# Kernel optimization log

Measured on AMD Instinct MI355X. Metric: run time of the kernel, lower is better.

## Reference

```python
import jax, jax.numpy as jnp
import numpy as np

P = 3          # graph partitions
CO = 64        # out_channels
KS = 9         # temporal kernel size (Gamma)
STRIDE = 1     # temporal stride
EPS = 1e-3     # keras BatchNormalization default epsilon


def setup_inputs() -> dict:
    key = jax.random.key(0)
    k1, k2, k3 = jax.random.split(key, 3)
    x = jax.random.normal(k1, (32, 64, 300, 25), dtype=jnp.float32)      # (N, C_in, L, V)
    A = jax.random.uniform(k2, (3, 25, 25), dtype=jnp.float32)           # (P, V, V)
    W = jax.random.normal(k3, (64, 192), dtype=jnp.float32) * 0.05       # (C_in, C_out*P)
    gamma = jnp.ones((64,), dtype=jnp.float32)
    beta = jnp.zeros((64,), dtype=jnp.float32)
    mean = jnp.zeros((64,), dtype=jnp.float32)
    var = jnp.ones((64,), dtype=jnp.float32)
    return {"x": x, "A": A, "W": W, "gamma": gamma, "beta": beta, "mean": mean, "var": var}


def _lt_matrix(L):
    # sum of shifted identities: lt[r, r + i*STRIDE] = 1 for i in [0, KS//STRIDE)
    lt = jnp.zeros((L, L), dtype=jnp.float32)
    for i in range(KS // STRIDE):
        lt = lt + jnp.eye(L, k=i * STRIDE, dtype=jnp.float32)
    return lt


def reference(x, A, W, gamma, beta, mean, var):
    N, C, L, V = x.shape
    res = x  # identity residual (in_channels == out_channels, stride == 1)
    # 1x1 conv: (N,C,L,V) x (C, CO*P) -> (N, CO*P, L, V); channel k = c*P + p (split into CO groups of P)
    y = jnp.einsum('nclv,ck->nklv', x, W)
    y = y.reshape(N, CO, P, L, V)  # (N, C_out, P, L, V)
    # partitioned graph matmul over joints: contract V with A[p]
    z = jnp.einsum('ncplv,pvw->ncplw', y, A)
    # temporal aggregation via handcrafted banded matrix, then sum over partitions
    lt = _lt_matrix(L)
    t = jnp.einsum('ncplv,lm->ncmv', z, lt)  # partition sum fused into einsum
    # BN (inference) over channel axis + ReLU
    inv = gamma / jnp.sqrt(var + EPS)
    xn = (t - mean[None, :, None, None]) * inv[None, :, None, None] + beta[None, :, None, None]
    xn = jax.nn.relu(xn)
    # residual add + final ReLU (dropout is identity at inference)
    return jax.nn.relu(xn + res)
```

## Files before the change

kernel.cpp:

```cpp
#include <hip/hip_runtime.h>
#include <cstdint>
#include <cstddef>

typedef short bf16x8 __attribute__((ext_vector_type(8)));
typedef float f32x4 __attribute__((ext_vector_type(4)));

#define EPS 1e-3f

__device__ __forceinline__ short f32_to_bf16s(float f) {
    union { float f; uint32_t u; } v; v.f = f;
    return (short)((v.u + 0x7FFFu + ((v.u >> 16) & 1u)) >> 16);
}

__global__ __launch_bounds__(256) void prep_kernel(const float* __restrict__ A,
                                                   const float* __restrict__ W,
                                                   unsigned short* __restrict__ wt,
                                                   unsigned short* __restrict__ at) {
    int idx = blockIdx.x * 256 + threadIdx.x;
    if (idx < 12288) {
        int kp = idx >> 6, ci = idx & 63;
        wt[idx] = (unsigned short)f32_to_bf16s(W[ci * 192 + kp]);
    } else {
        int j = idx - 12288;
        if (j < 3072) {
            int w = j / 96, k = j - w * 96;
            float val = 0.f;
            if (w < 25 && k < 75) {
                int p = k / 25, v = k - p * 25;
                val = A[(p * 25 + v) * 25 + w];
            }
            at[j] = (unsigned short)f32_to_bf16s(val);
        }
    }
}

__device__ __forceinline__ void do_group(int g, const unsigned short* __restrict__ wt,
    short* smem, const bf16x8 (&b1)[2][2], const bf16x8 (&b2)[2][3],
    const float* __restrict__ xn, float* __restrict__ outn,
    const float* scs, const float* shs,
    int lg, int wv, int q, int lcol)
{
    bf16x8 a1[3][2];
    #pragma unroll
    for (int mt = 0; mt < 3; ++mt)
        #pragma unroll
        for (int s = 0; s < 2; ++s)
            a1[mt][s] = *(const bf16x8*)(wt + (size_t)(g * 48 + mt * 16 + lcol) * 64 + 32 * s + 8 * q);

    f32x4 acc[3][2];
    #pragma unroll
    for (int mt = 0; mt < 3; ++mt)
        #pragma unroll
        for (int nt = 0; nt < 2; ++nt) acc[mt][nt] = (f32x4){0.f, 0.f, 0.f, 0.f};
    #pragma unroll
    for (int s = 0; s < 2; ++s)
        #pragma unroll
        for (int mt = 0; mt < 3; ++mt) {
            bf16x8 av = a1[mt][s];
            #pragma unroll
            for (int nt = 0; nt < 2; ++nt)
                acc[mt][nt] = __builtin_amdgcn_mfma_f32_16x16x32_bf16(av, b1[nt][s], acc[mt][nt], 0, 0, 0);
        }

    const size_t rbase = (size_t)lg * 25;
    float res[2][4];
    #pragma unroll
    for (int nt = 0; nt < 2; ++nt) {
        int w = nt * 16 + lcol;
        bool val = (w < 25) && (lg < 300);
        #pragma unroll
        for (int r = 0; r < 4; ++r) {
            int c = g * 16 + 4 * q + r;
            res[nt][r] = val ? xn[rbase + (size_t)c * 7500 + w] : 0.f;
        }
    }

    #pragma unroll
    for (int mt = 0; mt < 3; ++mt)
        #pragma unroll
        for (int nt = 0; nt < 2; ++nt) {
            int v = nt * 16 + lcol;
            if (v < 25) {
                #pragma unroll
                for (int r = 0; r < 4; ++r) {
                    int kpl = mt * 16 + 4 * q + r;
                    int cl = kpl / 3, p = kpl - 3 * cl;
                    smem[(wv * 16 + cl) * 104 + 25 * p + v] = f32_to_bf16s(acc[mt][nt][r]);
                }
            }
        }

    f32x4 c0 = {0.f, 0.f, 0.f, 0.f}, c1 = {0.f, 0.f, 0.f, 0.f};
    #pragma unroll
    for (int s = 0; s < 3; ++s) {
        bf16x8 a2 = *(const bf16x8*)&smem[(wv * 16 + lcol) * 104 + 32 * s + 8 * q];
        c0 = __builtin_amdgcn_mfma_f32_16x16x32_bf16(a2, b2[0][s], c0, 0, 0, 0);
        c1 = __builtin_amdgcn_mfma_f32_16x16x32_bf16(a2, b2[1][s], c1, 0, 0, 0);
    }

    if (lg < 300) {
        #pragma unroll
        for (int nt = 0; nt < 2; ++nt) {
            int w = nt * 16 + lcol;
            if (w < 25) {
                f32x4 cc = nt ? c1 : c0;
                #pragma unroll
                for (int r = 0; r < 4; ++r) {
                    int c = g * 16 + 4 * q + r;
                    float o = fmaxf(cc[r] * scs[c] + shs[c], 0.f);
                    __builtin_nontemporal_store(fmaxf(o + res[nt][r], 0.f),
                                                &outn[rbase + (size_t)c * 7500 + w]);
                }
            }
        }
    }
}

__device__ __forceinline__ void process_sample(
    const float* __restrict__ xn, float* __restrict__ outn,
    const unsigned short* __restrict__ wt,
    short* smem, const bf16x8 (&b2)[2][3],
    const float* scs, const float* shs,
    int l0, int tid, int wv, int lane, int q, int lcol)
{
    #pragma unroll 1
    for (int rep = 0; rep < 4; ++rep) {
        int cidx = tid + rep * 512;
        if (cidx < 1600) {
            int ci = cidx / 25, v = cidx - ci * 25;
            const float* xp = xn + (size_t)ci * 7500 + v;
            float vals[16];
            #pragma unroll
            for (int i = 0; i < 16; ++i) {
                int l = l0 - 8 + i;
                vals[i] = (l >= 0 && l < 300) ? xp[l * 25] : 0.f;
            }
            float run = vals[0] + vals[1] + vals[2] + vals[3]
                      + vals[4] + vals[5] + vals[6] + vals[7];
            short* wb = &smem[(ci >> 3) * 1656 + (ci & 7)];
            #pragma unroll
            for (int j = 0; j < 8; ++j) {
                run += vals[j + 8];
                wb[(j * 25 + v) * 8] = f32_to_bf16s(run);
                run -= vals[j];
            }
        }
    }
    __syncthreads();

    bf16x8 b1[2][2];
    #pragma unroll
    for (int nt = 0; nt < 2; ++nt) {
        int col = wv * 25 + nt * 16 + lcol;
        #pragma unroll
        for (int s = 0; s < 2; ++s)
            b1[nt][s] = *(const bf16x8*)&smem[(4 * s + q) * 1656 + col * 8];
    }
    __syncthreads();

    #pragma unroll
    for (int i = lane; i < 512; i += 64) {
        int r = i >> 5, cc = 72 + (i & 31);
        smem[(wv * 16 + r) * 104 + cc] = 0;
    }

    const int lg = l0 + wv;
    #pragma unroll 1
    for (int g = 0; g < 4; ++g)
        do_group(g, wt, smem, b1, b2, xn, outn, scs, shs, lg, wv, q, lcol);
}

__global__ __launch_bounds__(512, 4) void mega_kernel(
    const float* __restrict__ x,
    const unsigned short* __restrict__ wt,
    const unsigned short* __restrict__ at,
    const float* __restrict__ gamma, const float* __restrict__ beta,
    const float* __restrict__ mean, const float* __restrict__ var,
    float* __restrict__ out) {
    const int lin = blockIdx.x + 38 * blockIdx.y;
    const int logical = (lin & 7) * 76 + (lin >> 3);
    const int ch = logical % 38;
    const int n0 = (logical / 38) * 2;

    const int l0 = ch * 8;
    const int tid = threadIdx.x;
    const int wv = tid >> 6, lane = tid & 63, q = lane >> 4, lcol = lane & 15;

    __shared__ __align__(16) short smem[13312];
    __shared__ float scs[64], shs[64];

    const float* xn0 = x + (size_t)n0 * 480000;
    float* outn0 = out + (size_t)n0 * 480000;

    bf16x8 b2[2][3];
    #pragma unroll
    for (int nt = 0; nt < 2; ++nt)
        #pragma unroll
        for (int s = 0; s < 3; ++s)
            b2[nt][s] = *(const bf16x8*)(at + (size_t)(nt * 16 + lcol) * 96 + 32 * s + 8 * q);
    if (tid < 64) {
        float sc = gamma[tid] * rsqrtf(var[tid] + EPS);
        scs[tid] = sc;
        shs[tid] = beta[tid] - mean[tid] * sc;
    }

    process_sample(xn0, outn0, wt, smem, b2, scs, shs, l0, tid, wv, lane, q, lcol);
    __syncthreads();
    process_sample(xn0 + 480000, outn0 + 480000, wt, smem, b2, scs, shs,
                   l0, tid, wv, lane, q, lcol);
}

extern "C" void kernel_launch(void* const* d_in, const int* in_sizes, int n_in,
                              void* d_out, int out_size, void* d_ws, size_t ws_size,
                              hipStream_t stream) {
    const float* x     = (const float*)d_in[0];
    const float* A     = (const float*)d_in[1];
    const float* W     = (const float*)d_in[2];
    const float* gamma = (const float*)d_in[3];
    const float* beta  = (const float*)d_in[4];
    const float* mean  = (const float*)d_in[5];
    const float* var   = (const float*)d_in[6];
    float* out = (float*)d_out;

    char* ws = (char*)d_ws;
    unsigned short* wt = (unsigned short*)ws;
    unsigned short* at = (unsigned short*)(ws + 24576);

    prep_kernel<<<60, 256, 0, stream>>>(A, W, wt, at);
    mega_kernel<<<dim3(38, 16), 512, 0, stream>>>(x, wt, at, gamma, beta, mean, var, out);
}
```

Measured before the change: 182.7 us.

## Process one sample per block, batch all input loads, use regular stores

```diff
diff --git a/kernel.cpp b/kernel.cpp
--- a/kernel.cpp
+++ b/kernel.cpp
@@ -108,66 +108,11 @@
                 for (int r = 0; r < 4; ++r) {
                     int c = g * 16 + 4 * q + r;
                     float o = fmaxf(cc[r] * scs[c] + shs[c], 0.f);
-                    __builtin_nontemporal_store(fmaxf(o + res[nt][r], 0.f),
-                                                &outn[rbase + (size_t)c * 7500 + w]);
+                    outn[rbase + (size_t)c * 7500 + w] = fmaxf(o + res[nt][r], 0.f);
                 }
             }
         }
     }
-}
-
-__device__ __forceinline__ void process_sample(
-    const float* __restrict__ xn, float* __restrict__ outn,
-    const unsigned short* __restrict__ wt,
-    short* smem, const bf16x8 (&b2)[2][3],
-    const float* scs, const float* shs,
-    int l0, int tid, int wv, int lane, int q, int lcol)
-{
-    #pragma unroll 1
-    for (int rep = 0; rep < 4; ++rep) {
-        int cidx = tid + rep * 512;
-        if (cidx < 1600) {
-            int ci = cidx / 25, v = cidx - ci * 25;
-            const float* xp = xn + (size_t)ci * 7500 + v;
-            float vals[16];
-            #pragma unroll
-            for (int i = 0; i < 16; ++i) {
-                int l = l0 - 8 + i;
-                vals[i] = (l >= 0 && l < 300) ? xp[l * 25] : 0.f;
-            }
-            float run = vals[0] + vals[1] + vals[2] + vals[3]
-                      + vals[4] + vals[5] + vals[6] + vals[7];
-            short* wb = &smem[(ci >> 3) * 1656 + (ci & 7)];
-            #pragma unroll
-            for (int j = 0; j < 8; ++j) {
-                run += vals[j + 8];
-                wb[(j * 25 + v) * 8] = f32_to_bf16s(run);
-                run -= vals[j];
-            }
-        }
-    }
-    __syncthreads();
-
-    bf16x8 b1[2][2];
-    #pragma unroll
-    for (int nt = 0; nt < 2; ++nt) {
-        int col = wv * 25 + nt * 16 + lcol;
-        #pragma unroll
-        for (int s = 0; s < 2; ++s)
-            b1[nt][s] = *(const bf16x8*)&smem[(4 * s + q) * 1656 + col * 8];
-    }
-    __syncthreads();
-
-    #pragma unroll
-    for (int i = lane; i < 512; i += 64) {
-        int r = i >> 5, cc = 72 + (i & 31);
-        smem[(wv * 16 + r) * 104 + cc] = 0;
-    }
-
-    const int lg = l0 + wv;
-    #pragma unroll 1
-    for (int g = 0; g < 4; ++g)
-        do_group(g, wt, smem, b1, b2, xn, outn, scs, shs, lg, wv, q, lcol);
 }
 
 __global__ __launch_bounds__(512, 4) void mega_kernel(
@@ -178,9 +123,9 @@
     const float* __restrict__ mean, const float* __restrict__ var,
     float* __restrict__ out) {
     const int lin = blockIdx.x + 38 * blockIdx.y;
-    const int logical = (lin & 7) * 76 + (lin >> 3);
+    const int logical = (lin & 7) * 152 + (lin >> 3);
     const int ch = logical % 38;
-    const int n0 = (logical / 38) * 2;
+    const int n  = logical / 38;
 
     const int l0 = ch * 8;
     const int tid = threadIdx.x;
@@ -189,25 +134,86 @@
     __shared__ __align__(16) short smem[13312];
     __shared__ float scs[64], shs[64];
 
-    const float* xn0 = x + (size_t)n0 * 480000;
-    float* outn0 = out + (size_t)n0 * 480000;
-
-    bf16x8 b2[2][3];
-    #pragma unroll
-    for (int nt = 0; nt < 2; ++nt)
-        #pragma unroll
-        for (int s = 0; s < 3; ++s)
-            b2[nt][s] = *(const bf16x8*)(at + (size_t)(nt * 16 + lcol) * 96 + 32 * s + 8 * q);
+    const float* xn  = x   + (size_t)n * 480000;
+    float*       outn = out + (size_t)n * 480000;
+
     if (tid < 64) {
         float sc = gamma[tid] * rsqrtf(var[tid] + EPS);
         scs[tid] = sc;
         shs[tid] = beta[tid] - mean[tid] * sc;
     }
 
-    process_sample(xn0, outn0, wt, smem, b2, scs, shs, l0, tid, wv, lane, q, lcol);
+    int  loff[16];
+    bool lok[16];
+    #pragma unroll
+    for (int i = 0; i < 16; ++i) {
+        int l = l0 - 8 + i;
+        lok[i]  = (l >= 0) && (l < 300);
+        loff[i] = (lok[i] ? l : 0) * 25;
+    }
+
+    float vals[4][16];
+    int civ[4], vvv[4];
+    bool act[4];
+    #pragma unroll
+    for (int r = 0; r < 4; ++r) {
+        int cidx = tid + r * 512;
+        act[r] = cidx < 1600;
+        int cc = act[r] ? cidx : 0;
+        int ci = cc / 25, v = cc - ci * 25;
+        civ[r] = ci; vvv[r] = v;
+        const float* xp = xn + (size_t)ci * 7500 + v;
+        #pragma unroll
+        for (int i = 0; i < 16; ++i) {
+            float t = xp[loff[i]];
+            vals[r][i] = (act[r] && lok[i]) ? t : 0.f;
+        }
+    }
+
+    #pragma unroll
+    for (int r = 0; r < 4; ++r) {
+        if (act[r]) {
+            int ci = civ[r], v = vvv[r];
+            float run = vals[r][0] + vals[r][1] + vals[r][2] + vals[r][3]
+                      + vals[r][4] + vals[r][5] + vals[r][6] + vals[r][7];
+            short* wb = &smem[(ci >> 3) * 1656 + (ci & 7)];
+            #pragma unroll
+            for (int j = 0; j < 8; ++j) {
+                run += vals[r][j + 8];
+                wb[(j * 25 + v) * 8] = f32_to_bf16s(run);
+                run -= vals[r][j];
+            }
+        }
+    }
     __syncthreads();
-    process_sample(xn0 + 480000, outn0 + 480000, wt, smem, b2, scs, shs,
-                   l0, tid, wv, lane, q, lcol);
+
+    bf16x8 b2[2][3];
+    #pragma unroll
+    for (int nt = 0; nt < 2; ++nt)
+        #pragma unroll
+        for (int s = 0; s < 3; ++s)
+            b2[nt][s] = *(const bf16x8*)(at + (size_t)(nt * 16 + lcol) * 96 + 32 * s + 8 * q);
+
+    bf16x8 b1[2][2];
+    #pragma unroll
+    for (int nt = 0; nt < 2; ++nt) {
+        int col = wv * 25 + nt * 16 + lcol;
+        #pragma unroll
+        for (int s = 0; s < 2; ++s)
+            b1[nt][s] = *(const bf16x8*)&smem[(4 * s + q) * 1656 + col * 8];
+    }
+    __syncthreads();
+
+    #pragma unroll
+    for (int i = lane; i < 512; i += 64) {
+        int r = i >> 5, cc = 72 + (i & 31);
+        smem[(wv * 16 + r) * 104 + cc] = 0;
+    }
+
+    const int lg = l0 + wv;
+    #pragma unroll 1
+    for (int g = 0; g < 4; ++g)
+        do_group(g, wt, smem, b1, b2, xn, outn, scs, shs, lg, wv, q, lcol);
 }
 
 extern "C" void kernel_launch(void* const* d_in, const int* in_sizes, int n_in,
@@ -227,5 +233,5 @@
     unsigned short* at = (unsigned short*)(ws + 24576);
 
     prep_kernel<<<60, 256, 0, stream>>>(A, W, wt, at);
-    mega_kernel<<<dim3(38, 16), 512, 0, stream>>>(x, wt, at, gamma, beta, mean, var, out);
-}
+    mega_kernel<<<dim3(38, 32), 512, 0, stream>>>(x, wt, at, gamma, beta, mean, var, out);
+}
```

Result: slower. 188.7 us (+3.3%).

## Prefetch second sample's input into separate LDS buffer while computing first

Applied to the files above, without the earlier changes.

```diff
diff --git a/kernel.cpp b/kernel.cpp
--- a/kernel.cpp
+++ b/kernel.cpp
@@ -34,6 +34,35 @@
     }
 }
 
+__device__ __forceinline__ void p1_issue(const float* __restrict__ xn, int l0, int cidx,
+                                         float* v16) {
+    bool act = cidx < 1600;
+    int cc = act ? cidx : 0;
+    int ci = cc / 25, v = cc - ci * 25;
+    const float* xp = xn + (size_t)ci * 7500 + v;
+    #pragma unroll
+    for (int i = 0; i < 16; ++i) {
+        int l = l0 - 8 + i;
+        v16[i] = (act && l >= 0 && l < 300) ? xp[l * 25] : 0.f;
+    }
+}
+
+__device__ __forceinline__ void p1_consume(short* __restrict__ xbuf, int cidx,
+                                           const float* v16) {
+    if (cidx < 1600) {
+        int ci = cidx / 25, v = cidx - ci * 25;
+        float run = v16[0] + v16[1] + v16[2] + v16[3]
+                  + v16[4] + v16[5] + v16[6] + v16[7];
+        short* wb = &xbuf[(ci >> 3) * 1656 + (ci & 7)];
+        #pragma unroll
+        for (int j = 0; j < 8; ++j) {
+            run += v16[j + 8];
+            wb[(j * 25 + v) * 8] = f32_to_bf16s(run);
+            run -= v16[j];
+        }
+    }
+}
+
 __device__ __forceinline__ void do_group(int g, const unsigned short* __restrict__ wt,
     short* smem, const bf16x8 (&b1)[2][2], const bf16x8 (&b2)[2][3],
     const float* __restrict__ xn, float* __restrict__ outn,
@@ -108,89 +137,34 @@
                 for (int r = 0; r < 4; ++r) {
                     int c = g * 16 + 4 * q + r;
                     float o = fmaxf(cc[r] * scs[c] + shs[c], 0.f);
-                    __builtin_nontemporal_store(fmaxf(o + res[nt][r], 0.f),
-                                                &outn[rbase + (size_t)c * 7500 + w]);
+                    outn[rbase + (size_t)c * 7500 + w] = fmaxf(o + res[nt][r], 0.f);
                 }
             }
         }
     }
 }
 
-__device__ __forceinline__ void process_sample(
-    const float* __restrict__ xn, float* __restrict__ outn,
-    const unsigned short* __restrict__ wt,
-    short* smem, const bf16x8 (&b2)[2][3],
-    const float* scs, const float* shs,
-    int l0, int tid, int wv, int lane, int q, int lcol)
-{
-    #pragma unroll 1
-    for (int rep = 0; rep < 4; ++rep) {
-        int cidx = tid + rep * 512;
-        if (cidx < 1600) {
-            int ci = cidx / 25, v = cidx - ci * 25;
-            const float* xp = xn + (size_t)ci * 7500 + v;
-            float vals[16];
-            #pragma unroll
-            for (int i = 0; i < 16; ++i) {
-                int l = l0 - 8 + i;
-                vals[i] = (l >= 0 && l < 300) ? xp[l * 25] : 0.f;
-            }
-            float run = vals[0] + vals[1] + vals[2] + vals[3]
-                      + vals[4] + vals[5] + vals[6] + vals[7];
-            short* wb = &smem[(ci >> 3) * 1656 + (ci & 7)];
-            #pragma unroll
-            for (int j = 0; j < 8; ++j) {
-                run += vals[j + 8];
-                wb[(j * 25 + v) * 8] = f32_to_bf16s(run);
-                run -= vals[j];
-            }
-        }
-    }
-    __syncthreads();
-
-    bf16x8 b1[2][2];
-    #pragma unroll
-    for (int nt = 0; nt < 2; ++nt) {
-        int col = wv * 25 + nt * 16 + lcol;
-        #pragma unroll
-        for (int s = 0; s < 2; ++s)
-            b1[nt][s] = *(const bf16x8*)&smem[(4 * s + q) * 1656 + col * 8];
-    }
-    __syncthreads();
-
-    #pragma unroll
-    for (int i = lane; i < 512; i += 64) {
-        int r = i >> 5, cc = 72 + (i & 31);
-        smem[(wv * 16 + r) * 104 + cc] = 0;
-    }
-
-    const int lg = l0 + wv;
-    #pragma unroll 1
-    for (int g = 0; g < 4; ++g)
-        do_group(g, wt, smem, b1, b2, xn, outn, scs, shs, lg, wv, q, lcol);
-}
-
-__global__ __launch_bounds__(512, 4) void mega_kernel(
+__global__ __launch_bounds__(512, 6) void mega_kernel(
     const float* __restrict__ x,
     const unsigned short* __restrict__ wt,
     const unsigned short* __restrict__ at,
     const float* __restrict__ gamma, const float* __restrict__ beta,
     const float* __restrict__ mean, const float* __restrict__ var,
     float* __restrict__ out) {
-    const int lin = blockIdx.x + 38 * blockIdx.y;
-    const int logical = (lin & 7) * 76 + (lin >> 3);
-    const int ch = logical % 38;
-    const int n0 = (logical / 38) * 2;
-
+    const int ch = blockIdx.x;
+    const int n0 = blockIdx.y * 2;
     const int l0 = ch * 8;
     const int tid = threadIdx.x;
     const int wv = tid >> 6, lane = tid & 63, q = lane >> 4, lcol = lane & 15;
 
-    __shared__ __align__(16) short smem[13312];
+    __shared__ __align__(16) short smem[26560];
     __shared__ float scs[64], shs[64];
+    short* X1 = smem + 13312;
 
     const float* xn0 = x + (size_t)n0 * 480000;
+    const float* xn1 = xn0 + 480000;
     float* outn0 = out + (size_t)n0 * 480000;
+    float* outn1 = outn0 + 480000;
 
     bf16x8 b2[2][3];
     #pragma unroll
@@ -204,10 +178,64 @@
         shs[tid] = beta[tid] - mean[tid] * sc;
     }
 
-    process_sample(xn0, outn0, wt, smem, b2, scs, shs, l0, tid, wv, lane, q, lcol);
+    #pragma unroll 1
+    for (int rep = 0; rep < 4; ++rep) {
+        int cidx = tid + rep * 512;
+        float t16[16];
+        p1_issue(xn0, l0, cidx, t16);
+        p1_consume(smem, cidx, t16);
+    }
     __syncthreads();
-    process_sample(xn0 + 480000, outn0 + 480000, wt, smem, b2, scs, shs,
-                   l0, tid, wv, lane, q, lcol);
+
+    bf16x8 b1[2][2];
+    #pragma unroll
+    for (int nt = 0; nt < 2; ++nt) {
+        int col = wv * 25 + nt * 16 + lcol;
+        #pragma unroll
+        for (int s = 0; s < 2; ++s)
+            b1[nt][s] = *(const bf16x8*)&smem[(4 * s + q) * 1656 + col * 8];
+    }
+    __syncthreads();
+
+    #pragma unroll
+    for (int i = lane; i < 512; i += 64) {
+        int r = i >> 5, cc = 72 + (i & 31);
+        smem[(wv * 16 + r) * 104 + cc] = 0;
+    }
+
+    const int lg = l0 + wv;
+
+    {
+        float v16[16];
+        p1_issue(xn1, l0, tid, v16);
+        do_group(0, wt, smem, b1, b2, xn0, outn0, scs, shs, lg, wv, q, lcol);
+        p1_consume(X1, tid, v16);
+
+        p1_issue(xn1, l0, tid + 512, v16);
+        do_group(1, wt, smem, b1, b2, xn0, outn0, scs, shs, lg, wv, q, lcol);
+        p1_consume(X1, tid + 512, v16);
+
+        p1_issue(xn1, l0, tid + 1024, v16);
+        do_group(2, wt, smem, b1, b2, xn0, outn0, scs, shs, lg, wv, q, lcol);
+        p1_consume(X1, tid + 1024, v16);
+
+        p1_issue(xn1, l0, tid + 1536, v16);
+        do_group(3, wt, smem, b1, b2, xn0, outn0, scs, shs, lg, wv, q, lcol);
+        p1_consume(X1, tid + 1536, v16);
+    }
+    __syncthreads();
+
+    #pragma unroll
+    for (int nt = 0; nt < 2; ++nt) {
+        int col = wv * 25 + nt * 16 + lcol;
+        #pragma unroll
+        for (int s = 0; s < 2; ++s)
+            b1[nt][s] = *(const bf16x8*)&X1[(4 * s + q) * 1656 + col * 8];
+    }
+
+    #pragma unroll 1
+    for (int g = 0; g < 4; ++g)
+        do_group(g, wt, smem, b1, b2, xn1, outn1, scs, shs, lg, wv, q, lcol);
 }
 
 extern "C" void kernel_launch(void* const* d_in, const int* in_sizes, int n_in,
```

Result: slower. 265.3 us (+45.2%).
